# Optimization experiments

Measured on AMD Instinct MI355X. Metric: run time of the kernel, lower is better.

Reference implementation:

```python
import jax, jax.numpy as jnp
import numpy as np

N, P, ENC = 64, 64, 1536   # batch, pixels (8*8), enc channels
T = 32                     # caption length
V, E, A, H = 10000, 512, 512, 512  # vocab, embd_dim, attn_dim, hidden


def setup_inputs() -> dict:
    key = jax.random.key(0)
    ks = jax.random.split(key, 20)
    s = lambda k, sh, sc: jax.random.normal(k, sh, dtype=jnp.float32) * sc
    inp = {
        "features": jax.random.normal(ks[0], (N, P, ENC), dtype=jnp.float32),
        "captions": jax.random.randint(ks[1], (N, T), 0, V),
        "embd_W": s(ks[2], (V, E), 0.02),
        "attn_token_W": s(ks[3], (A, H), 0.02),
        "attn_token_b": jnp.zeros((A,), jnp.float32),
        "attn_feat_W": s(ks[4], (A, ENC), 0.02),
        "attn_feat_b": jnp.zeros((A,), jnp.float32),
        "attn_full_W": s(ks[5], (1, A), 0.02),
        "attn_full_b": jnp.zeros((1,), jnp.float32),
        "W_ih": s(ks[6], (4 * H, E + ENC), 0.02),  # LSTMCell input weights, gate order i,f,g,o
        "b_ih": jnp.zeros((4 * H,), jnp.float32),
        "W_hh": s(ks[7], (4 * H, H), 0.02),
        "b_hh": jnp.zeros((4 * H,), jnp.float32),
        "fc_W": s(ks[8], (V, H), 0.02),
        "fc_b": jnp.zeros((V,), jnp.float32),
        "init_Wh": s(ks[9], (P * ENC, H), 1.0 / np.sqrt(P * ENC)),  # torch.randn projection (scaled for stability)
        "init_Wc": s(ks[10], (P * ENC, H), 1.0 / np.sqrt(P * ENC)),
    }
    return inp


def reference(features, captions, embd_W, attn_token_W, attn_token_b,
              attn_feat_W, attn_feat_b, attn_full_W, attn_full_b,
              W_ih, b_ih, W_hh, b_hh, fc_W, fc_b, init_Wh, init_Wc):
    n = features.shape[0]
    # precompute attention projection of features once (hoisted; math identical)
    attn_img = jnp.einsum('npc,ac->npa', features, attn_feat_W) + attn_feat_b  # (N,P,A)
    embd_tokens = embd_W[captions].transpose(1, 0, 2)  # (T,N,E)

    h0 = features.reshape(n, -1) @ init_Wh  # (N,H)
    c0 = features.reshape(n, -1) @ init_Wc

    def step(carry, emb_t):
        h, c = carry
        # additive attention
        attn_h = h @ attn_token_W.T + attn_token_b              # (N,A)
        e = jax.nn.relu(attn_h[:, None, :] + attn_img)          # (N,P,A)
        logits = jax.nn.softmax(jnp.einsum('npa,oa->np', e, attn_full_W) + attn_full_b[0], axis=1)
        ctx = jnp.einsum('npc,np->nc', features, logits)        # (N,ENC)
        x_t = jnp.concatenate([ctx, emb_t], axis=1)             # (N,ENC+E)
        # LSTMCell (torch gate order i,f,g,o)
        gates = x_t @ W_ih.T + b_ih + h @ W_hh.T + b_hh
        i, f, g, o = jnp.split(gates, 4, axis=1)
        c_new = jax.nn.sigmoid(f) * c + jax.nn.sigmoid(i) * jnp.tanh(g)
        h_new = jax.nn.sigmoid(o) * jnp.tanh(c_new)
        return (h_new, c_new), h_new

    # note: concat order in original is (attn_ctx, embd); preserved above
    (_, _), h_out = jax.lax.scan(step, (h0, c0), embd_tokens)   # h_out: (T,N,H)
    preds = (h_out @ fc_W.T + fc_b).transpose(1, 0, 2)          # (N,T,V); dropout = identity (eval)
    return preds
```

## Files before the change

### kernel.cpp

```cpp
#include <hip/hip_runtime.h>

__device__ __forceinline__ float sigf(float x) { return 1.0f / (1.0f + __expf(-x)); }

__global__ void __launch_bounds__(256) transpose_kernel(
    const float* __restrict__ in, float* __restrict__ out, int R, int C, int out_ld)
{
    __shared__ float tl[32][33];
    int tx = threadIdx.x, ty = threadIdx.y;
    int c0 = blockIdx.x * 32, r0 = blockIdx.y * 32;
#pragma unroll
    for (int i = 0; i < 4; i++) {
        int r = r0 + ty + i * 8, c = c0 + tx;
        if (r < R && c < C) tl[ty + i * 8][tx] = in[(size_t)r * C + c];
    }
    __syncthreads();
#pragma unroll
    for (int i = 0; i < 4; i++) {
        int c = c0 + ty + i * 8, r = r0 + tx;
        if (r < R && c < C) out[(size_t)c * out_ld + r] = tl[tx][ty + i * 8];
    }
}

__global__ void __launch_bounds__(256) prep_bcomb(const float* __restrict__ b_ih,
                                                  const float* __restrict__ b_hh,
                                                  float* __restrict__ bcomb)
{
    int i = blockIdx.x * 256 + threadIdx.x;
    if (i < 2048) bcomb[i] = b_ih[i] + b_hh[i];
}

template <int GATHER, int REMAP>
__global__ void __launch_bounds__(256) gemm_nt(
    const float* __restrict__ A, int lda, const float* __restrict__ B, int ldb,
    const int* __restrict__ caps, const float* __restrict__ bias,
    float* __restrict__ C, int ldc, int J, int K)
{
    __shared__ float la[32 * 132];
    __shared__ float lb[32 * 68];
    const int tid = threadIdx.x;
    const int m0 = blockIdx.x * 128, j0 = blockIdx.y * 64;
    const int tx = tid & 15, ty = tid >> 4;
    float acc[8][4] = {};

    for (int k0 = 0; k0 < K; k0 += 32) {
        __syncthreads();
        {
            int r0 = tid >> 3, c4 = (tid & 7) * 4;
#pragma unroll
            for (int p = 0; p < 4; p++) {
                int m = m0 + r0 + p * 32;
                int arow = GATHER ? caps[(m & 63) * 32 + (m >> 6)] : m;
                const float4 v = *(const float4*)&A[(size_t)arow * lda + k0 + c4];
#pragma unroll
                for (int q = 0; q < 4; q++) la[(c4 + q) * 132 + r0 + p * 32] = ((const float*)&v)[q];
            }
        }
        {
            int r0 = tid >> 3, c4 = (tid & 7) * 4;
#pragma unroll
            for (int p = 0; p < 2; p++) {
                int j = j0 + r0 + p * 32;
                if (j >= J) j = J - 1;
                const float4 v = *(const float4*)&B[(size_t)j * ldb + k0 + c4];
#pragma unroll
                for (int q = 0; q < 4; q++) lb[(c4 + q) * 68 + r0 + p * 32] = ((const float*)&v)[q];
            }
        }
        __syncthreads();
#pragma unroll
        for (int kk = 0; kk < 32; kk++) {
            float bv[4];
            *(float4*)bv = *(const float4*)&lb[kk * 68 + tx * 4];
#pragma unroll
            for (int pi = 0; pi < 2; pi++) {
                float av[4];
                *(float4*)av = *(const float4*)&la[kk * 132 + ty * 8 + pi * 4];
#pragma unroll
                for (int i = 0; i < 4; i++)
#pragma unroll
                    for (int jj = 0; jj < 4; jj++)
                        acc[pi * 4 + i][jj] += av[i] * bv[jj];
            }
        }
    }
    const int j = j0 + tx * 4;
#pragma unroll
    for (int pi = 0; pi < 2; pi++)
#pragma unroll
        for (int i = 0; i < 4; i++) {
            int m = m0 + ty * 8 + pi * 4 + i;
            int orow = REMAP ? ((m & 63) * 32 + (m >> 6)) : m;
#pragma unroll
            for (int jj = 0; jj < 4; jj++)
                if (j + jj < J)
                    C[(size_t)orow * ldc + j + jj] = acc[pi * 4 + i][jj] + bias[j + jj];
        }
}

__global__ void __launch_bounds__(256) init_gemm(
    const float* __restrict__ features, const float* __restrict__ Wh,
    const float* __restrict__ Wc, float* __restrict__ ipart)
{
    __shared__ float la[32 * 68];
    __shared__ float lb[32 * 68];
    const int tid = threadIdx.x;
    const int jg0 = blockIdx.x * 64, kc = blockIdx.y;
    const float* Bsrc = (jg0 < 512) ? Wh : Wc;
    const int j0 = (jg0 < 512) ? jg0 : jg0 - 512;
    const int tx = tid & 15, ty = tid >> 4;
    float acc[4][4] = {};

    for (int kt = 0; kt < 64; kt++) {
        const int k0 = kc * 2048 + kt * 32;
        __syncthreads();
        {
            int r0 = tid >> 3, c4 = (tid & 7) * 4;
#pragma unroll
            for (int p = 0; p < 2; p++) {
                const float4 v = *(const float4*)&features[(size_t)(r0 + p * 32) * 98304 + k0 + c4];
#pragma unroll
                for (int q = 0; q < 4; q++) la[(c4 + q) * 68 + r0 + p * 32] = ((const float*)&v)[q];
            }
        }
        {
            int kr = tid >> 4, j4 = (tid & 15) * 4;
#pragma unroll
            for (int p = 0; p < 2; p++) {
                const float4 v = *(const float4*)&Bsrc[(size_t)(k0 + kr + p * 16) * 512 + j0 + j4];
                *(float4*)&lb[(kr + p * 16) * 68 + j4] = v;
            }
        }
        __syncthreads();
#pragma unroll
        for (int kk = 0; kk < 32; kk++) {
            float av[4], bv[4];
            *(float4*)av = *(const float4*)&la[kk * 68 + ty * 4];
            *(float4*)bv = *(const float4*)&lb[kk * 68 + tx * 4];
#pragma unroll
            for (int i = 0; i < 4; i++)
#pragma unroll
                for (int jj = 0; jj < 4; jj++) acc[i][jj] += av[i] * bv[jj];
        }
    }
#pragma unroll
    for (int i = 0; i < 4; i++) {
        int m = ty * 4 + i;
#pragma unroll
        for (int jj = 0; jj < 4; jj++)
            ipart[(size_t)(kc * 64 + m) * 1024 + jg0 + tx * 4 + jj] = acc[i][jj];
    }
}

__global__ void __launch_bounds__(256) init_reduce(const float* __restrict__ ipart,
                                                   float* __restrict__ xh,
                                                   float* __restrict__ cbuf)
{
    int idx = blockIdx.x * 256 + threadIdx.x;
    int n = idx >> 10, jg = idx & 1023;
    float s = 0.0f;
#pragma unroll 8
    for (int kc = 0; kc < 48; kc++) s += ipart[(size_t)(kc * 64 + n) * 1024 + jg];
    if (jg < 512) xh[(size_t)n * 2048 + 1536 + jg] = s;
    else          cbuf[(size_t)n * 512 + (jg - 512)] = s;
}

__global__ void __launch_bounds__(256) gates_gemm(
    const float* __restrict__ xh, const float* __restrict__ W_ih,
    const float* __restrict__ W_hh, float* __restrict__ gpart)
{
    __shared__ float la[32 * 68];
    __shared__ float lb[32 * 68];
    const int tid = threadIdx.x;
    const int j0 = blockIdx.x * 64, kc = blockIdx.y;
    const int tx = tid & 15, ty = tid >> 4;
    float acc[4][4] = {};

    for (int kt = 0; kt < 8; kt++) {
        const int k0 = kc * 256 + kt * 32;
        __syncthreads();
        {
            int r0 = tid >> 3, c4 = (tid & 7) * 4;
#pragma unroll
            for (int p = 0; p < 2; p++) {
                const float4 v = *(const float4*)&xh[(size_t)(r0 + p * 32) * 2048 + k0 + c4];
#pragma unroll
                for (int q = 0; q < 4; q++) la[(c4 + q) * 68 + r0 + p * 32] = ((const float*)&v)[q];
            }
        }
        {
            int r0 = tid >> 3, c4 = (tid & 7) * 4;
#pragma unroll
            for (int p = 0; p < 2; p++) {
                int j = j0 + r0 + p * 32;
                const float* src = (k0 < 1536) ? &W_ih[(size_t)j * 2048 + k0 + c4]
                                               : &W_hh[(size_t)j * 512 + (k0 - 1536) + c4];
                const float4 v = *(const float4*)src;
#pragma unroll
                for (int q = 0; q < 4; q++) lb[(c4 + q) * 68 + r0 + p * 32] = ((const float*)&v)[q];
            }
        }
        __syncthreads();
#pragma unroll
        for (int kk = 0; kk < 32; kk++) {
            float av[4], bv[4];
            *(float4*)av = *(const float4*)&la[kk * 68 + ty * 4];
            *(float4*)bv = *(const float4*)&lb[kk * 68 + tx * 4];
#pragma unroll
            for (int i = 0; i < 4; i++)
#pragma unroll
                for (int jj = 0; jj < 4; jj++) acc[i][jj] += av[i] * bv[jj];
        }
    }
#pragma unroll
    for (int i = 0; i < 4; i++) {
        int m = ty * 4 + i;
#pragma unroll
        for (int jj = 0; jj < 4; jj++)
            gpart[(size_t)(kc * 64 + m) * 2048 + j0 + tx * 4 + jj] = acc[i][jj];
    }
}

__global__ void __launch_bounds__(256) attn_step_kernel(
    const float* __restrict__ features, const float* __restrict__ attn_img,
    const float* __restrict__ AtkWT, const float* __restrict__ atk_b,
    const float* __restrict__ full_W, const float* __restrict__ full_b,
    const float* __restrict__ emb_part, const float* __restrict__ gpart,
    float* __restrict__ xh, float* __restrict__ cbuf, float* __restrict__ h_out, int t)
{
    __shared__ float lds_h[512];
    __shared__ float lds_ah[512];
    __shared__ float lds_fw[512];
    __shared__ float lds_red[256];
    __shared__ float lds_logit[64];

    const int n = blockIdx.x, tid = threadIdx.x;
    const int wid = tid >> 6, lane = tid & 63;

    if (t > 0) {
        for (int hh = tid; hh < 512; hh += 256) {
            float g[4];
#pragma unroll
            for (int q = 0; q < 4; q++) {
                float s = emb_part[(size_t)((t - 1) * 64 + n) * 2048 + q * 512 + hh];
#pragma unroll
                for (int kc = 0; kc < 8; kc++)
                    s += gpart[(size_t)(kc * 64 + n) * 2048 + q * 512 + hh];
                g[q] = s;
            }
            float cold = cbuf[(size_t)n * 512 + hh];
            float cn = sigf(g[1]) * cold + sigf(g[0]) * tanhf(g[2]);
            float hn = sigf(g[3]) * tanhf(cn);
            cbuf[(size_t)n * 512 + hh] = cn;
            xh[(size_t)n * 2048 + 1536 + hh] = hn;
            h_out[(size_t)((t - 1) * 64 + n) * 512 + hh] = hn;
            lds_h[hh] = hn;
        }
    } else {
        for (int hh = tid; hh < 512; hh += 256) lds_h[hh] = xh[(size_t)n * 2048 + 1536 + hh];
    }
    for (int k = tid; k < 512; k += 256) lds_fw[k] = full_W[k];
    __syncthreads();

    {
        float a0 = atk_b[tid], a1 = atk_b[tid + 256];
#pragma unroll 4
        for (int k = 0; k < 512; k++) {
            float hk = lds_h[k];
            a0 += hk * AtkWT[(size_t)k * 512 + tid];
            a1 += hk * AtkWT[(size_t)k * 512 + tid + 256];
        }
        lds_ah[tid] = a0;
        lds_ah[tid + 256] = a1;
    }
    __syncthreads();

    for (int p = 0; p < 64; p++) {
        const float* img = attn_img + (size_t)(n * 64 + p) * 512;
        float e0 = fmaxf(lds_ah[tid] + img[tid], 0.0f);
        float e1 = fmaxf(lds_ah[tid + 256] + img[tid + 256], 0.0f);
        float part = e0 * lds_fw[tid] + e1 * lds_fw[tid + 256];
#pragma unroll
        for (int off = 32; off > 0; off >>= 1) part += __shfl_down(part, off, 64);
        if (lane == 0) lds_red[p * 4 + wid] = part;
    }
    __syncthreads();

    if (tid < 64) {
        float s = lds_red[tid * 4] + lds_red[tid * 4 + 1] + lds_red[tid * 4 + 2] +
                  lds_red[tid * 4 + 3] + full_b[0];
        float m = s;
#pragma unroll
        for (int off = 32; off > 0; off >>= 1) m = fmaxf(m, __shfl_xor(m, off, 64));
        float e = __expf(s - m);
        float sum = e;
#pragma unroll
        for (int off = 32; off > 0; off >>= 1) sum += __shfl_xor(sum, off, 64);
        lds_logit[tid] = e / sum;
    }
    __syncthreads();

    for (int cc = tid; cc < 1536; cc += 256) {
        const float* f = features + (size_t)(n * 64) * 1536 + cc;
        float acc = 0.0f;
#pragma unroll 8
        for (int p = 0; p < 64; p++) acc += lds_logit[p] * f[(size_t)p * 1536];
        xh[(size_t)n * 2048 + cc] = acc;
    }
}

__global__ void __launch_bounds__(256) final_update_kernel(
    const float* __restrict__ gpart, const float* __restrict__ emb_part,
    const float* __restrict__ cbuf, float* __restrict__ h_out)
{
    int idx = blockIdx.x * 256 + threadIdx.x;
    int n = idx >> 9, hh = idx & 511;
    float g[4];
#pragma unroll
    for (int q = 0; q < 4; q++) {
        float s = emb_part[(size_t)(31 * 64 + n) * 2048 + q * 512 + hh];
#pragma unroll
        for (int kc = 0; kc < 8; kc++)
            s += gpart[(size_t)(kc * 64 + n) * 2048 + q * 512 + hh];
        g[q] = s;
    }
    float cold = cbuf[(size_t)n * 512 + hh];
    float cn = sigf(g[1]) * cold + sigf(g[0]) * tanhf(g[2]);
    float hn = sigf(g[3]) * tanhf(cn);
    h_out[(size_t)(31 * 64 + n) * 512 + hh] = hn;
}

extern "C" void kernel_launch(void* const* d_in, const int* in_sizes, int n_in,
                              void* d_out, int out_size, void* d_ws, size_t ws_size,
                              hipStream_t stream)
{
    const float* features = (const float*)d_in[0];
    const int*   captions = (const int*)d_in[1];
    const float* embd_W   = (const float*)d_in[2];
    const float* atk_W    = (const float*)d_in[3];
    const float* atk_b    = (const float*)d_in[4];
    const float* af_W     = (const float*)d_in[5];
    const float* af_b     = (const float*)d_in[6];
    const float* full_W   = (const float*)d_in[7];
    const float* full_b   = (const float*)d_in[8];
    const float* W_ih     = (const float*)d_in[9];
    const float* b_ih     = (const float*)d_in[10];
    const float* W_hh     = (const float*)d_in[11];
    const float* b_hh     = (const float*)d_in[12];
    const float* fc_W     = (const float*)d_in[13];
    const float* fc_b     = (const float*)d_in[14];
    const float* init_Wh  = (const float*)d_in[15];
    const float* init_Wc  = (const float*)d_in[16];
    float* out = (float*)d_out;

    float* ws = (float*)d_ws;
    float* AtkWT    = ws; ws += 512 * 512;
    float* bcomb    = ws; ws += 2048;
    float* attn_img = ws; ws += 4096 * 512;
    float* emb_part = ws; ws += 2048 * 2048;
    float* ipart    = ws; ws += 48 * 64 * 1024;
    float* xh       = ws; ws += 64 * 2048;
    float* cbuf     = ws; ws += 64 * 512;
    float* gpart    = ws; ws += 8 * 64 * 2048;
    float* h_out    = ws; ws += 2048 * 512;

    transpose_kernel<<<dim3(16, 16), dim3(32, 8), 0, stream>>>(atk_W, AtkWT, 512, 512, 512);
    prep_bcomb<<<8, 256, 0, stream>>>(b_ih, b_hh, bcomb);

    gemm_nt<0, 0><<<dim3(32, 8), 256, 0, stream>>>(
        features, 1536, af_W, 1536, nullptr, af_b, attn_img, 512, 512, 1536);
    gemm_nt<1, 0><<<dim3(16, 32), 256, 0, stream>>>(
        embd_W, 512, W_ih + 1536, 2048, captions, bcomb, emb_part, 2048, 2048, 512);
    init_gemm<<<dim3(16, 48), 256, 0, stream>>>(features, init_Wh, init_Wc, ipart);
    init_reduce<<<256, 256, 0, stream>>>(ipart, xh, cbuf);

    for (int t = 0; t < 32; t++) {
        attn_step_kernel<<<64, 256, 0, stream>>>(features, attn_img, AtkWT, atk_b,
                                                 full_W, full_b, emb_part, gpart,
                                                 xh, cbuf, h_out, t);
        gates_gemm<<<dim3(32, 8), 256, 0, stream>>>(xh, W_ih, W_hh, gpart);
    }
    final_update_kernel<<<128, 256, 0, stream>>>(gpart, emb_part, cbuf, h_out);

    gemm_nt<0, 1><<<dim3(16, 157), 256, 0, stream>>>(
        h_out, 512, fc_W, 512, nullptr, fc_b, out, 10000, 10000, 512);
}
```

Measured before the change: 4.357 ms.

## Fuse recurrent loop into one persistent cooperative kernel with grid syncs

Replaces the 64 per-timestep launches of the attention and gates kernels, plus the final update, with a single cooperative kernel of 256 blocks of 1024 threads that loops over time and uses grid.sync between phases. The gates GEMM now splits K over 4 thread groups per block, producing 32 partial sums instead of 8, and prefetches the next tile into registers. The attention step is also spread across 1024 threads. This removes launch overhead and adds more partial-sum reduction work. Only 64 of the 256 blocks do the attention phase, and grid-wide barriers bring their own latency.

New measurement: 4.167 ms. 1.05x faster.

```diff
diff --git a/kernel.cpp b/kernel.cpp
--- a/kernel.cpp
+++ b/kernel.cpp
@@ -1,4 +1,7 @@
 #include <hip/hip_runtime.h>
+#include <hip/hip_cooperative_groups.h>
+
+namespace cg = cooperative_groups;
 
 __device__ __forceinline__ float sigf(float x) { return 1.0f / (1.0f + __expf(-x)); }
 
@@ -164,169 +167,176 @@
     else          cbuf[(size_t)n * 512 + (jg - 512)] = s;
 }
 
-__global__ void __launch_bounds__(256) gates_gemm(
-    const float* __restrict__ xh, const float* __restrict__ W_ih,
-    const float* __restrict__ W_hh, float* __restrict__ gpart)
-{
-    __shared__ float la[32 * 68];
-    __shared__ float lb[32 * 68];
-    const int tid = threadIdx.x;
-    const int j0 = blockIdx.x * 64, kc = blockIdx.y;
-    const int tx = tid & 15, ty = tid >> 4;
-    float acc[4][4] = {};
-
-    for (int kt = 0; kt < 8; kt++) {
-        const int k0 = kc * 256 + kt * 32;
-        __syncthreads();
-        {
-            int r0 = tid >> 3, c4 = (tid & 7) * 4;
-#pragma unroll
-            for (int p = 0; p < 2; p++) {
-                const float4 v = *(const float4*)&xh[(size_t)(r0 + p * 32) * 2048 + k0 + c4];
-#pragma unroll
-                for (int q = 0; q < 4; q++) la[(c4 + q) * 68 + r0 + p * 32] = ((const float*)&v)[q];
-            }
-        }
-        {
-            int r0 = tid >> 3, c4 = (tid & 7) * 4;
-#pragma unroll
-            for (int p = 0; p < 2; p++) {
-                int j = j0 + r0 + p * 32;
-                const float* src = (k0 < 1536) ? &W_ih[(size_t)j * 2048 + k0 + c4]
-                                               : &W_hh[(size_t)j * 512 + (k0 - 1536) + c4];
-                const float4 v = *(const float4*)src;
-#pragma unroll
-                for (int q = 0; q < 4; q++) lb[(c4 + q) * 68 + r0 + p * 32] = ((const float*)&v)[q];
-            }
-        }
-        __syncthreads();
-#pragma unroll
-        for (int kk = 0; kk < 32; kk++) {
-            float av[4], bv[4];
-            *(float4*)av = *(const float4*)&la[kk * 68 + ty * 4];
-            *(float4*)bv = *(const float4*)&lb[kk * 68 + tx * 4];
-#pragma unroll
-            for (int i = 0; i < 4; i++)
-#pragma unroll
-                for (int jj = 0; jj < 4; jj++) acc[i][jj] += av[i] * bv[jj];
-        }
-    }
-#pragma unroll
-    for (int i = 0; i < 4; i++) {
-        int m = ty * 4 + i;
-#pragma unroll
-        for (int jj = 0; jj < 4; jj++)
-            gpart[(size_t)(kc * 64 + m) * 2048 + j0 + tx * 4 + jj] = acc[i][jj];
-    }
-}
-
-__global__ void __launch_bounds__(256) attn_step_kernel(
+__global__ void __launch_bounds__(1024) loop_kernel(
     const float* __restrict__ features, const float* __restrict__ attn_img,
     const float* __restrict__ AtkWT, const float* __restrict__ atk_b,
     const float* __restrict__ full_W, const float* __restrict__ full_b,
-    const float* __restrict__ emb_part, const float* __restrict__ gpart,
-    float* __restrict__ xh, float* __restrict__ cbuf, float* __restrict__ h_out, int t)
-{
+    const float* __restrict__ emb_part, const float* __restrict__ W_ih,
+    const float* __restrict__ W_hh, float* __restrict__ gpart,
+    float* __restrict__ xh, float* __restrict__ cbuf, float* __restrict__ h_out)
+{
+    __shared__ float la[32 * 68];
+    __shared__ float lb[32 * 68];
     __shared__ float lds_h[512];
     __shared__ float lds_ah[512];
     __shared__ float lds_fw[512];
-    __shared__ float lds_red[256];
+    __shared__ float lds_red[64];
     __shared__ float lds_logit[64];
-
-    const int n = blockIdx.x, tid = threadIdx.x;
-    const int wid = tid >> 6, lane = tid & 63;
-
-    if (t > 0) {
-        for (int hh = tid; hh < 512; hh += 256) {
-            float g[4];
-#pragma unroll
-            for (int q = 0; q < 4; q++) {
-                float s = emb_part[(size_t)((t - 1) * 64 + n) * 2048 + q * 512 + hh];
-#pragma unroll
-                for (int kc = 0; kc < 8; kc++)
-                    s += gpart[(size_t)(kc * 64 + n) * 2048 + q * 512 + hh];
-                g[q] = s;
-            }
-            float cold = cbuf[(size_t)n * 512 + hh];
-            float cn = sigf(g[1]) * cold + sigf(g[0]) * tanhf(g[2]);
-            float hn = sigf(g[3]) * tanhf(cn);
-            cbuf[(size_t)n * 512 + hh] = cn;
-            xh[(size_t)n * 2048 + 1536 + hh] = hn;
-            h_out[(size_t)((t - 1) * 64 + n) * 512 + hh] = hn;
-            lds_h[hh] = hn;
-        }
-    } else {
-        for (int hh = tid; hh < 512; hh += 256) lds_h[hh] = xh[(size_t)n * 2048 + 1536 + hh];
-    }
-    for (int k = tid; k < 512; k += 256) lds_fw[k] = full_W[k];
-    __syncthreads();
-
-    {
-        float a0 = atk_b[tid], a1 = atk_b[tid + 256];
-#pragma unroll 4
-        for (int k = 0; k < 512; k++) {
-            float hk = lds_h[k];
-            a0 += hk * AtkWT[(size_t)k * 512 + tid];
-            a1 += hk * AtkWT[(size_t)k * 512 + tid + 256];
-        }
-        lds_ah[tid] = a0;
-        lds_ah[tid + 256] = a1;
-    }
-    __syncthreads();
-
-    for (int p = 0; p < 64; p++) {
-        const float* img = attn_img + (size_t)(n * 64 + p) * 512;
-        float e0 = fmaxf(lds_ah[tid] + img[tid], 0.0f);
-        float e1 = fmaxf(lds_ah[tid + 256] + img[tid + 256], 0.0f);
-        float part = e0 * lds_fw[tid] + e1 * lds_fw[tid + 256];
-#pragma unroll
-        for (int off = 32; off > 0; off >>= 1) part += __shfl_down(part, off, 64);
-        if (lane == 0) lds_red[p * 4 + wid] = part;
-    }
-    __syncthreads();
-
-    if (tid < 64) {
-        float s = lds_red[tid * 4] + lds_red[tid * 4 + 1] + lds_red[tid * 4 + 2] +
-                  lds_red[tid * 4 + 3] + full_b[0];
-        float m = s;
-#pragma unroll
-        for (int off = 32; off > 0; off >>= 1) m = fmaxf(m, __shfl_xor(m, off, 64));
-        float e = __expf(s - m);
-        float sum = e;
-#pragma unroll
-        for (int off = 32; off > 0; off >>= 1) sum += __shfl_xor(sum, off, 64);
-        lds_logit[tid] = e / sum;
-    }
-    __syncthreads();
-
-    for (int cc = tid; cc < 1536; cc += 256) {
-        const float* f = features + (size_t)(n * 64) * 1536 + cc;
-        float acc = 0.0f;
+    __shared__ float gbuf[2048];
+
+    cg::grid_group grid = cg::this_grid();
+    const int blk = blockIdx.x, tid = threadIdx.x;
+    const int n = blk;
+    const int jt = blk >> 3, kc = blk & 7;
+    const int j0 = jt * 64;
+    const int gq = tid >> 8, ltid = tid & 255;
+    const int tx = ltid & 15, ty = ltid >> 4;
+    const int sr = tid >> 4, skk2 = (tid & 15) * 2;
+
+    if (blk < 64 && tid < 512) lds_fw[tid] = full_W[tid];
+
+    for (int t = 0; t < 32; ++t) {
+        if (blk < 64) {
+            if (t > 0) {
+                for (int idx = tid; idx < 2048; idx += 1024) {
+                    float s = emb_part[(size_t)((t - 1) * 64 + n) * 2048 + idx];
 #pragma unroll 8
-        for (int p = 0; p < 64; p++) acc += lds_logit[p] * f[(size_t)p * 1536];
-        xh[(size_t)n * 2048 + cc] = acc;
-    }
-}
-
-__global__ void __launch_bounds__(256) final_update_kernel(
-    const float* __restrict__ gpart, const float* __restrict__ emb_part,
-    const float* __restrict__ cbuf, float* __restrict__ h_out)
-{
-    int idx = blockIdx.x * 256 + threadIdx.x;
-    int n = idx >> 9, hh = idx & 511;
-    float g[4];
-#pragma unroll
-    for (int q = 0; q < 4; q++) {
-        float s = emb_part[(size_t)(31 * 64 + n) * 2048 + q * 512 + hh];
-#pragma unroll
-        for (int kc = 0; kc < 8; kc++)
-            s += gpart[(size_t)(kc * 64 + n) * 2048 + q * 512 + hh];
-        g[q] = s;
-    }
-    float cold = cbuf[(size_t)n * 512 + hh];
-    float cn = sigf(g[1]) * cold + sigf(g[0]) * tanhf(g[2]);
-    float hn = sigf(g[3]) * tanhf(cn);
-    h_out[(size_t)(31 * 64 + n) * 512 + hh] = hn;
+                    for (int s32 = 0; s32 < 32; s32++)
+                        s += gpart[(size_t)(s32 * 64 + n) * 2048 + idx];
+                    gbuf[idx] = s;
+                }
+                __syncthreads();
+                if (tid < 512) {
+                    float cold = cbuf[(size_t)n * 512 + tid];
+                    float cn = sigf(gbuf[512 + tid]) * cold + sigf(gbuf[tid]) * tanhf(gbuf[1024 + tid]);
+                    float hn = sigf(gbuf[1536 + tid]) * tanhf(cn);
+                    cbuf[(size_t)n * 512 + tid] = cn;
+                    xh[(size_t)n * 2048 + 1536 + tid] = hn;
+                    h_out[(size_t)((t - 1) * 64 + n) * 512 + tid] = hn;
+                    lds_h[tid] = hn;
+                }
+            } else {
+                if (tid < 512) lds_h[tid] = xh[(size_t)n * 2048 + 1536 + tid];
+            }
+            __syncthreads();
+
+            {
+                const int a = tid & 511, half = tid >> 9;
+                const float* col = AtkWT + (size_t)(half * 256) * 512 + a;
+                const float* hp = lds_h + half * 256;
+                float s = 0.0f;
+#pragma unroll 8
+                for (int k = 0; k < 256; k++) s += hp[k] * col[(size_t)k * 512];
+                gbuf[half * 512 + a] = s;
+            }
+            __syncthreads();
+            if (tid < 512) lds_ah[tid] = atk_b[tid] + gbuf[tid] + gbuf[512 + tid];
+            __syncthreads();
+
+            {
+                const int w = tid >> 6, lane = tid & 63;
+#pragma unroll
+                for (int i = 0; i < 4; i++) {
+                    const int p = i * 16 + w;
+                    const float* img = attn_img + (size_t)(n * 64 + p) * 512;
+                    float part = 0.0f;
+#pragma unroll
+                    for (int jx = 0; jx < 8; jx++) {
+                        int a = lane + jx * 64;
+                        part += fmaxf(lds_ah[a] + img[a], 0.0f) * lds_fw[a];
+                    }
+#pragma unroll
+                    for (int off = 32; off > 0; off >>= 1) part += __shfl_down(part, off, 64);
+                    if (lane == 0) lds_red[p] = part;
+                }
+            }
+            __syncthreads();
+
+            if (tid < 64) {
+                float s = lds_red[tid] + full_b[0];
+                float m = s;
+#pragma unroll
+                for (int off = 32; off > 0; off >>= 1) m = fmaxf(m, __shfl_xor(m, off, 64));
+                float e = __expf(s - m);
+                float sum = e;
+#pragma unroll
+                for (int off = 32; off > 0; off >>= 1) sum += __shfl_xor(sum, off, 64);
+                lds_logit[tid] = e / sum;
+            }
+            __syncthreads();
+
+            for (int cc = tid; cc < 1536; cc += 1024) {
+                const float* f = features + (size_t)(n * 64) * 1536 + cc;
+                float acc = 0.0f;
+#pragma unroll 16
+                for (int p = 0; p < 64; p++) acc += lds_logit[p] * f[(size_t)p * 1536];
+                xh[(size_t)n * 2048 + cc] = acc;
+            }
+        }
+        grid.sync();
+
+        {
+            float acc[4][4] = {};
+            float2 pa, pb;
+            {
+                const int k0 = kc * 256;
+                pa = *(const float2*)&xh[(size_t)sr * 2048 + k0 + skk2];
+                const int kg = k0 + skk2;
+                const float* src = (kg < 1536) ? &W_ih[(size_t)(j0 + sr) * 2048 + kg]
+                                               : &W_hh[(size_t)(j0 + sr) * 512 + kg - 1536];
+                pb = *(const float2*)src;
+            }
+            for (int kt = 0; kt < 8; kt++) {
+                __syncthreads();
+                la[skk2 * 68 + sr] = pa.x; la[(skk2 + 1) * 68 + sr] = pa.y;
+                lb[skk2 * 68 + sr] = pb.x; lb[(skk2 + 1) * 68 + sr] = pb.y;
+                if (kt < 7) {
+                    const int k0 = kc * 256 + (kt + 1) * 32;
+                    pa = *(const float2*)&xh[(size_t)sr * 2048 + k0 + skk2];
+                    const int kg = k0 + skk2;
+                    const float* src = (kg < 1536) ? &W_ih[(size_t)(j0 + sr) * 2048 + kg]
+                                                   : &W_hh[(size_t)(j0 + sr) * 512 + kg - 1536];
+                    pb = *(const float2*)src;
+                }
+                __syncthreads();
+#pragma unroll
+                for (int kq = 0; kq < 8; kq++) {
+                    const int kk = gq * 8 + kq;
+                    float av[4], bv[4];
+                    *(float4*)av = *(const float4*)&la[kk * 68 + ty * 4];
+                    *(float4*)bv = *(const float4*)&lb[kk * 68 + tx * 4];
+#pragma unroll
+                    for (int i = 0; i < 4; i++)
+#pragma unroll
+                        for (int jj = 0; jj < 4; jj++) acc[i][jj] += av[i] * bv[jj];
+                }
+            }
+#pragma unroll
+            for (int i = 0; i < 4; i++)
+#pragma unroll
+                for (int jj = 0; jj < 4; jj++)
+                    gpart[(size_t)((kc * 4 + gq) * 64 + ty * 4 + i) * 2048 + j0 + tx * 4 + jj]
+                        = acc[i][jj];
+        }
+        grid.sync();
+    }
+
+    if (blk < 64) {
+        for (int idx = tid; idx < 2048; idx += 1024) {
+            float s = emb_part[(size_t)(31 * 64 + n) * 2048 + idx];
+#pragma unroll 8
+            for (int s32 = 0; s32 < 32; s32++)
+                s += gpart[(size_t)(s32 * 64 + n) * 2048 + idx];
+            gbuf[idx] = s;
+        }
+        __syncthreads();
+        if (tid < 512) {
+            float cold = cbuf[(size_t)n * 512 + tid];
+            float cn = sigf(gbuf[512 + tid]) * cold + sigf(gbuf[tid]) * tanhf(gbuf[1024 + tid]);
+            float hn = sigf(gbuf[1536 + tid]) * tanhf(cn);
+            h_out[(size_t)(31 * 64 + n) * 512 + tid] = hn;
+        }
+    }
 }
 
 extern "C" void kernel_launch(void* const* d_in, const int* in_sizes, int n_in,
@@ -357,10 +367,10 @@
     float* bcomb    = ws; ws += 2048;
     float* attn_img = ws; ws += 4096 * 512;
     float* emb_part = ws; ws += 2048 * 2048;
-    float* ipart    = ws; ws += 48 * 64 * 1024;
+    float* gpart    = ws;
+    float* ipart    = ws; ws += 32 * 64 * 2048;
     float* xh       = ws; ws += 64 * 2048;
     float* cbuf     = ws; ws += 64 * 512;
-    float* gpart    = ws; ws += 8 * 64 * 2048;
     float* h_out    = ws; ws += 2048 * 512;
 
     transpose_kernel<<<dim3(16, 16), dim3(32, 8), 0, stream>>>(atk_W, AtkWT, 512, 512, 512);
@@ -373,13 +383,15 @@
     init_gemm<<<dim3(16, 48), 256, 0, stream>>>(features, init_Wh, init_Wc, ipart);
     init_reduce<<<256, 256, 0, stream>>>(ipart, xh, cbuf);
 
-    for (int t = 0; t < 32; t++) {
-        attn_step_kernel<<<64, 256, 0, stream>>>(features, attn_img, AtkWT, atk_b,
-                                                 full_W, full_b, emb_part, gpart,
-                                                 xh, cbuf, h_out, t);
-        gates_gemm<<<dim3(32, 8), 256, 0, stream>>>(xh, W_ih, W_hh, gpart);
-    }
-    final_update_kernel<<<128, 256, 0, stream>>>(gpart, emb_part, cbuf, h_out);
+    {
+        void* kargs[] = {
+            (void*)&features, (void*)&attn_img, (void*)&AtkWT, (void*)&atk_b,
+            (void*)&full_W, (void*)&full_b, (void*)&emb_part, (void*)&W_ih,
+            (void*)&W_hh, (void*)&gpart, (void*)&xh, (void*)&cbuf, (void*)&h_out
+        };
+        hipLaunchCooperativeKernel((void*)loop_kernel, dim3(256), dim3(1024),
+                                   kargs, 0, stream);
+    }
 
     gemm_nt<0, 1><<<dim3(16, 157), 256, 0, stream>>>(
         h_out, 512, fc_W, 512, nullptr, fc_b, out, 10000, 10000, 512);
```
